# Performance work log

Hardware: AMD Instinct MI355X
Metric: run time of the kernel (lower is better)

## Reference

```python
import jax, jax.numpy as jnp
import numpy as np

N_NODES, N_EDGES, N_REL, F_DIM, N_HEAD, N_LAYERS = 20000, 100000, 1000, 128, 4, 4
NEG_SLOPE = 0.2  # PyG GATv2Conv default negative_slope


def _gatv2_layer(x, ea_full, src, dst, Wl, bl, Wr, br, We, att, bias):
    # x: [N, F]; ea_full: [Etot, F] edge attrs (incl. self-loop rows)
    N = x.shape[0]
    H, C = att.shape  # heads, out-dim per head
    xl = (x @ Wl + bl).reshape(N, H, C)          # source-side projection
    xr = (x @ Wr + br).reshape(N, H, C)          # target-side projection
    ee = (ea_full @ We).reshape(-1, H, C)        # [Etot, H, C] edge embedding
    # GATv2 scoring: leaky_relu(x_i + x_j + e) . att
    e = jax.nn.leaky_relu(xl[src] + xr[dst] + ee, NEG_SLOPE)
    logits = jnp.einsum('ehc,hc->eh', e, att)    # [Etot, H]
    # segment softmax over edges grouped by destination node
    m = jax.ops.segment_max(logits, dst, num_segments=N)
    p = jnp.exp(logits - m[dst])
    denom = jax.ops.segment_sum(p, dst, num_segments=N)
    alpha = p / denom[dst]                       # [Etot, H]
    out = jax.ops.segment_sum(alpha[:, :, None] * xl[src], dst, num_segments=N)
    return out.mean(axis=1) + bias               # concat=False -> head mean


def setup_inputs() -> dict:
    key = jax.random.key(0)
    ks = jax.random.split(key, 12)
    N, E, R, F, H, L = N_NODES, N_EDGES, N_REL, F_DIM, N_HEAD, N_LAYERS
    HC = H * F
    s = 1.0 / np.sqrt(F)
    return {
        'x': jax.random.normal(ks[0], (N, F), jnp.float32),
        'edge_index': jax.random.randint(ks[1], (2, E), 0, N, dtype=jnp.int32),
        'relations': jax.random.normal(ks[2], (R, F), jnp.float32),
        'relation_index': jax.random.randint(ks[3], (E,), 0, R, dtype=jnp.int32),
        'Wl': jax.random.normal(ks[4], (L, F, HC), jnp.float32) * s,
        'bl': jnp.zeros((L, HC), jnp.float32),
        'Wr': jax.random.normal(ks[5], (L, F, HC), jnp.float32) * s,
        'br': jnp.zeros((L, HC), jnp.float32),
        'We': jax.random.normal(ks[6], (L, F, HC), jnp.float32) * s,
        'att': jax.random.normal(ks[7], (L, H, F), jnp.float32) * s,
        'bias': jnp.zeros((L, F), jnp.float32),
    }


def reference(x, edge_index, relations, relation_index, Wl, bl, Wr, br, We, att, bias):
    N = x.shape[0]
    sl = jnp.arange(N, dtype=edge_index.dtype)
    src = jnp.concatenate([edge_index[0], sl])   # add_self_loops=True
    dst = jnp.concatenate([edge_index[1], sl])
    ea = relations[relation_index]               # [E, F]
    # self-loop edge_attr uses fill_value='mean' (PyG default)
    ea_mean = ea.mean(axis=0)
    ea_full = jnp.concatenate([ea, jnp.broadcast_to(ea_mean, (N, ea.shape[1]))])
    h = x
    for l in range(N_LAYERS):
        h = _gatv2_layer(h, ea_full, src, dst, Wl[l], bl[l], Wr[l], br[l], We[l], att[l], bias[l])
    return (h, relations)
```

## Files before the change

kernel.cpp:

```cpp
#include <hip/hip_runtime.h>
#include <hip/hip_bf16.h>

#define N_NODES   20000
#define N_EDGES   100000
#define N_REL     1000
#define F_DIM     128
#define N_HEAD    4
#define HC        512
#define HC2       256
#define N_LAYERS  4
#define REL_EXT_ROWS 1008
#define NEG_SLOPE 0.2f
#define PROJ_NODE_X 79

typedef __attribute__((ext_vector_type(8))) short short8;
typedef __attribute__((ext_vector_type(4))) float floatx4;

__device__ __forceinline__ float loadIn(const void* p, size_t i, int f32) {
    if (f32) return ((const float*)p)[i];
    union { unsigned int u; float f; } c;
    c.u = ((unsigned int)((const unsigned short*)p)[i]) << 16;
    return c.f;
}

__device__ __forceinline__ unsigned short f2bf(float v) {
    __hip_bfloat16 b = __float2bfloat16(v);
    return *(unsigned short*)&b;
}

__device__ __forceinline__ void unpack2(unsigned int u, float& lo, float& hi) {
    union { unsigned int u; float f; } a, b;
    a.u = u << 16;
    b.u = u & 0xFFFF0000u;
    lo = a.f; hi = b.f;
}

__device__ __forceinline__ void unpack8(uint4 v, float* f) {
    unpack2(v.x, f[0], f[1]);
    unpack2(v.y, f[2], f[3]);
    unpack2(v.z, f[4], f[5]);
    unpack2(v.w, f[6], f[7]);
}

__device__ __forceinline__ void gload_lds16(const unsigned short* g, short* l) {
    __builtin_amdgcn_global_load_lds(
        (const __attribute__((address_space(1))) unsigned int*)g,
        (__attribute__((address_space(3))) unsigned int*)l,
        16, 0, 0);
}

__global__ void detect_kernel(const unsigned short* __restrict__ x, int* __restrict__ flag) {
    int t = threadIdx.x;
    int cnt = 0;
    for (int j = t; j < 256; j += 64) {
        int e = (x[j] >> 7) & 0xFF;
        if (e >= 143) cnt++;
    }
    for (int off = 32; off; off >>= 1) cnt += __shfl_xor(cnt, off);
    if (t == 0) flag[0] = (cnt >= 8) ? 1 : 0;
}

__global__ void xcast_kernel(const void* __restrict__ x, unsigned short* __restrict__ xbf,
                             const int* __restrict__ flag) {
    int idx = blockIdx.x * 256 + threadIdx.x;
    if (idx >= N_NODES * F_DIM / 4) return;
    int f32 = flag[0];
    uint2 o;
    if (f32) {
        float4 v = ((const float4*)x)[idx];
        o.x = (unsigned int)f2bf(v.x) | ((unsigned int)f2bf(v.y) << 16);
        o.y = (unsigned int)f2bf(v.z) | ((unsigned int)f2bf(v.w) << 16);
    } else {
        o = ((const uint2*)x)[idx];
    }
    ((uint2*)xbf)[idx] = o;
}


__global__ void hist_kernel(const int* __restrict__ dst, const int* __restrict__ rel,
                            int* __restrict__ deg, int* __restrict__ rcount) {
    int e = blockIdx.x * 256 + threadIdx.x;
    if (e < N_EDGES) {
        atomicAdd(&deg[dst[e]], 1);
        atomicAdd(&rcount[rel[e]], 1);
    }
}

__global__ void ea_mean_kernel(const int* __restrict__ rcount,
                               const void* __restrict__ relations,
                               float* __restrict__ ea_mean, const int* __restrict__ flag) {
    int f32 = flag[0];
    int b = blockIdx.x;
    int t = threadIdx.x;
    int col = t & 127;
    int rhalf = t >> 7;
    float acc = 0.f;
    for (int j = 0; j < 4; ++j) {
        int r = b * 8 + j * 2 + rhalf;
        acc += (float)rcount[r] * loadIn(relations, (size_t)r * F_DIM + col, f32);
    }
    __shared__ float part[256];
    part[t] = acc;
    __syncthreads();
    if (t < 128)
        atomicAdd(&ea_mean[col], (part[t] + part[t + 128]) * (1.f / (float)N_EDGES));
}

__global__ void relext_kernel(const void* __restrict__ relations,
                              const float* __restrict__ ea_mean,
                              unsigned short* __restrict__ rel_ext, const int* __restrict__ flag) {
    int idx = blockIdx.x * 256 + threadIdx.x;
    if (idx >= REL_EXT_ROWS * F_DIM) return;
    int f32 = flag[0];
    int r = idx >> 7;
    int c = idx & 127;
    float v;
    if (r < N_REL)       v = loadIn(relations, idx, f32);
    else if (r == N_REL) v = ea_mean[c];
    else                 v = 0.f;
    rel_ext[idx] = f2bf(v);
}

__global__ void scan_kernel(const int* __restrict__ deg,
                            int* __restrict__ row_start, int* __restrict__ cursor) {
    __shared__ int part[1024];
    int t = threadIdx.x;
    const int CH = (N_NODES + 1023) / 1024;
    int base = t * CH;
    int sum = 0;
    for (int j = 0; j < CH; ++j) {
        int idx = base + j;
        if (idx < N_NODES) sum += deg[idx];
    }
    part[t] = sum;
    __syncthreads();
    for (int off = 1; off < 1024; off <<= 1) {
        int u = (t >= off) ? part[t - off] : 0;
        __syncthreads();
        part[t] += u;
        __syncthreads();
    }
    int run = part[t] - sum;
    for (int j = 0; j < CH; ++j) {
        int idx = base + j;
        if (idx < N_NODES) {
            row_start[idx] = run;
            cursor[idx] = run;
            run += deg[idx];
        }
    }
    if (t == 1023) row_start[N_NODES] = part[1023];
}

__global__ void scatter_kernel(const int* __restrict__ src, const int* __restrict__ dst,
                               const int* __restrict__ rel, int* __restrict__ cursor,
                               int* __restrict__ csr_pack) {
    int e = blockIdx.x * 256 + threadIdx.x;
    if (e < N_EDGES) {
        int d = dst[e];
        int p = atomicAdd(&cursor[d], 1);
        csr_pack[p] = src[e] | (rel[e] << 16);
    }
}

__global__ void build8_kernel(const int* __restrict__ row_start,
                              const int* __restrict__ csr_pack,
                              int* __restrict__ csr8) {
    int i = blockIdx.x * 256 + threadIdx.x;
    if (i >= N_NODES) return;
    int rs = row_start[i];
    int deg = row_start[i + 1] - rs;
    if (deg < 0) deg = 0;
    int dcap = deg > 4095 ? 4095 : deg;
    csr8[i * 8] = rs | (dcap << 17);
    #pragma unroll
    for (int k = 0; k < 7; ++k)
        csr8[i * 8 + 1 + k] = (k < deg) ? csr_pack[rs + k] : 0;
}

__global__ void tail_kernel(const void* __restrict__ relations, void* __restrict__ out,
                            const int* __restrict__ flag) {
    int i = blockIdx.x * 256 + threadIdx.x;
    if (i >= N_REL * F_DIM) return;
    int f32 = flag[0];
    float v = loadIn(relations, i, f32);
    size_t o = (size_t)N_NODES * F_DIM + i;
    if (f32) ((float*)out)[o] = v;
    else     ((unsigned short*)out)[o] = f2bf(v);
}

__global__ void w_transpose_kernel(const void* __restrict__ Wl, const void* __restrict__ Wr,
                                   const void* __restrict__ We,
                                   unsigned short* __restrict__ Wt, const int* __restrict__ flag) {
    int f32 = flag[0];
    int k0 = blockIdx.x * 64;
    int n0 = blockIdx.y * 64;
    int mat = blockIdx.z;
    const void* src = (mat < 4) ? Wl : (mat < 8 ? Wr : We);
    size_t base = (size_t)(mat & 3) * F_DIM * HC;
    unsigned short* dst = Wt + (size_t)mat * HC * F_DIM;
    __shared__ float T[64][65];
    int t = threadIdx.x;
    int r = t >> 2, cq = t & 3;
    for (int j = 0; j < 16; ++j) {
        int n = cq * 16 + j;
        T[n][r] = loadIn(src, base + (size_t)(k0 + r) * HC + n0 + n, f32);
    }
    __syncthreads();
    for (int j = 0; j < 16; ++j) {
        int k = cq * 16 + j;
        dst[(size_t)(n0 + r) * F_DIM + k0 + k] = f2bf(T[r][k]);
    }
}

__launch_bounds__(256, 2)
__global__ void proj_kernel(const unsigned short* __restrict__ A_node,
                            const unsigned short* __restrict__ rel_ext,
                            const unsigned short* __restrict__ Wlt,
                            const unsigned short* __restrict__ Wrt,
                            const unsigned short* __restrict__ Wet,
                            const void* __restrict__ bl, const void* __restrict__ br,
                            size_t boff,
                            unsigned short* __restrict__ xl,
                            unsigned short* __restrict__ xr,
                            unsigned short* __restrict__ re,
                            const int* __restrict__ flag) {
    __shared__ __align__(16) short As[2][64 * 128];
    __shared__ __align__(16) short Cw[4][32][72];
    int f32 = flag[0];
    int t = threadIdx.x;
    int y = blockIdx.y;
    int isNode = (blockIdx.x < PROJ_NODE_X);

    const unsigned short* A;
    const unsigned short* WtM[2];
    const void* biasM[2];
    unsigned short* outM[2];
    int M, mbase, n0M[2];
    if (isNode) {
        A = A_node; M = N_NODES;
        mbase = blockIdx.x * 256;
        WtM[0] = Wlt;  WtM[1] = Wrt;
        biasM[0] = bl; biasM[1] = br;
        outM[0] = xl;  outM[1] = xr;
        n0M[0] = y * 128; n0M[1] = y * 128;
    } else {
        A = rel_ext; M = REL_EXT_ROWS;
        int s = (blockIdx.x - PROJ_NODE_X) * 4 + y;
        mbase = (s >> 1) * 256;
        WtM[0] = Wet;  WtM[1] = Wet;
        biasM[0] = nullptr; biasM[1] = nullptr;
        outM[0] = re;  outM[1] = re;
        n0M[0] = (s & 1) * 256; n0M[1] = (s & 1) * 256 + 128;
    }
    const int nT = 4;

    int wave = t >> 6, lane = t & 63;
    int wm = (wave >> 1) * 32, wn = (wave & 1) * 64;
    int r16 = lane & 15, quad = lane >> 4;

    short8 breg[2][2][2][4];
    #pragma unroll
    for (int m = 0; m < 2; ++m)
        #pragma unroll
        for (int half = 0; half < 2; ++half)
            #pragma unroll
            for (int kk = 0; kk < 2; ++kk)
                #pragma unroll
                for (int ni = 0; ni < 4; ++ni)
                    breg[m][half][kk][ni] = *(const short8*)(
                        WtM[m] + (size_t)(n0M[m] + wn + ni * 16 + r16) * F_DIM
                               + half * 64 + kk * 32 + quad * 8);

    float bvv[2][4];
    #pragma unroll
    for (int m = 0; m < 2; ++m)
        #pragma unroll
        for (int ni = 0; ni < 4; ++ni)
            bvv[m][ni] = biasM[m] ? loadIn(biasM[m], boff + n0M[m] + wn + ni * 16 + r16, f32) : 0.f;

    auto STAGE = [&](int buf, int ct2) {
        int base = mbase + ct2 * 64;
        #pragma unroll
        for (int j = 0; j < 4; ++j) {
            int c = t + j * 256;
            int row = c >> 4, ch = c & 15;
            int gm = base + row;
            if (gm >= M) gm = M - 1;
            int sch = ch ^ (row & 15);
            gload_lds16(A + (size_t)gm * F_DIM + sch * 8, &As[buf][c * 8]);
        }
    };

    STAGE(0, 0);
    asm volatile("s_waitcnt vmcnt(0)" ::: "memory");
    __builtin_amdgcn_sched_barrier(0);
    __syncthreads();

    int cur = 0;
    for (int ct = 0; ct < nT; ++ct) {
        int m0 = mbase + ct * 64;
        if (ct + 1 < nT) STAGE(cur ^ 1, ct + 1);
        __builtin_amdgcn_sched_barrier(0);

        short8 afr[2][2][2];
        #pragma unroll
        for (int half = 0; half < 2; ++half)
            #pragma unroll
            for (int kk = 0; kk < 2; ++kk)
                #pragma unroll
                for (int mi = 0; mi < 2; ++mi) {
                    int row = wm + mi * 16 + r16;
                    int pch = (half * 8 + kk * 4 + quad) ^ (row & 15);
                    afr[half][kk][mi] = *(const short8*)&As[cur][row * 128 + pch * 8];
                }

        #pragma unroll
        for (int m = 0; m < 2; ++m) {
            floatx4 acc[2][4];
            #pragma unroll
            for (int mi = 0; mi < 2; ++mi)
                #pragma unroll
                for (int ni = 0; ni < 4; ++ni)
                    acc[mi][ni] = (floatx4){0.f, 0.f, 0.f, 0.f};

            #pragma unroll
            for (int half = 0; half < 2; ++half)
                #pragma unroll
                for (int kk = 0; kk < 2; ++kk)
                    #pragma unroll
                    for (int mi = 0; mi < 2; ++mi)
                        #pragma unroll
                        for (int ni = 0; ni < 4; ++ni)
                            acc[mi][ni] = __builtin_amdgcn_mfma_f32_16x16x32_bf16(
                                afr[half][kk][mi], breg[m][half][kk][ni], acc[mi][ni], 0, 0, 0);

            #pragma unroll
            for (int mi = 0; mi < 2; ++mi)
                #pragma unroll
                for (int ni = 0; ni < 4; ++ni)
                    #pragma unroll
                    for (int r = 0; r < 4; ++r)
                        Cw[wave][mi * 16 + quad * 4 + r][ni * 16 + r16] =
                            (short)f2bf(acc[mi][ni][r] + bvv[m][ni]);
            asm volatile("s_waitcnt lgkmcnt(0)" ::: "memory");
            __builtin_amdgcn_sched_barrier(0);

            unsigned short* out = outM[m];
            #pragma unroll
            for (int j = 0; j < 4; ++j) {
                int c = j * 64 + lane;
                int lr = c >> 3, chunk = c & 7;
                int gm = m0 + wm + lr;
                if (gm >= M) gm = M - 1;
                *(short8*)(out + (size_t)gm * HC + n0M[m] + wn + chunk * 8) =
                    *(const short8*)&Cw[wave][lr][chunk * 8];
            }
        }

        if (ct + 1 < nT) {
            asm volatile("s_waitcnt vmcnt(8)" ::: "memory");
            __builtin_amdgcn_sched_barrier(0);
        }
        __builtin_amdgcn_s_barrier();
        cur ^= 1;
    }
}

__launch_bounds__(128)
__global__ void edge_kernel(const unsigned int* __restrict__ xl2,
                            const unsigned int* __restrict__ xr2,
                            const unsigned int* __restrict__ re2,
                            const int* __restrict__ csr8,
                            const int* __restrict__ csr_pack,
                            const void* __restrict__ att, size_t att_off,
                            const void* __restrict__ bias, size_t bias_off,
                            void* __restrict__ hout, int final_layer,
                            const int* __restrict__ flag) {
    int f32 = flag[0];
    int wid = threadIdx.x >> 6;
    int lane = threadIdx.x & 63;
    int i = blockIdx.x * 2 + wid;
    if (i >= N_NODES) return;
    int h = lane >> 4;
    int q = lane & 15;
    int loff = h * 64 + q * 4;

    uint4 h0 = *(const uint4*)(csr8 + (size_t)i * 8);
    uint4 h1 = *(const uint4*)(csr8 + (size_t)i * 8 + 4);
    int rs  = (int)(h0.x & 0x1FFFF);
    int deg = (int)(h0.x >> 17) & 0xFFF;
    int ew[7] = { (int)h0.y, (int)h0.z, (int)h0.w, (int)h1.x, (int)h1.y, (int)h1.z, (int)h1.w };

    float xr[8];
    { uint4 v = *(const uint4*)(xr2 + (size_t)i * HC2 + loff); unpack8(v, xr); }
    float er[8];
    { uint4 v = *(const uint4*)(re2 + (size_t)N_REL * HC2 + loff); unpack8(v, er); }
    float av[8];
    #pragma unroll
    for (int j = 0; j < 8; ++j)
        av[j] = loadIn(att, att_off + (size_t)h * F_DIM + q * 8 + j, f32);

    int nIn = deg > 7 ? 7 : deg;
    uint4 xv[7], rv[7];
    #pragma unroll
    for (int k = 0; k < 7; ++k) {
        if (k < nIn) {
            int pk = ew[k];
            int sn = pk & 0xFFFF;        if (sn >= N_NODES) sn = 0;
            int rn = (pk >> 16) & 0x3FF; if (rn > N_REL) rn = N_REL;
            xv[k] = *(const uint4*)(xl2 + (size_t)sn * HC2 + loff);
            rv[k] = *(const uint4*)(re2 + (size_t)rn * HC2 + loff);
        }
    }

    float acc[8];
    float s;
    {
        float xs[8];
        uint4 v = *(const uint4*)(xl2 + (size_t)i * HC2 + loff);
        unpack8(v, xs);
        float part = 0.f;
        #pragma unroll
        for (int j = 0; j < 8; ++j) {
            float u = xs[j] + xr[j] + er[j];
            u = fmaxf(u, NEG_SLOPE * u);
            part = fmaf(u, av[j], part);
        }
        #pragma unroll
        for (int off = 8; off; off >>= 1) part += __shfl_xor(part, off);
        part = fminf(fmaxf(part, -60.f), 60.f);
        float p = __expf(part);
        s = p;
        #pragma unroll
        for (int j = 0; j < 8; ++j) acc[j] = p * xs[j];
    }

    #pragma unroll
    for (int k = 0; k < 7; ++k) {
        if (k < nIn) {
            float xlv[8], ee[8];
            unpack8(xv[k], xlv);
            unpack8(rv[k], ee);
            float part = 0.f;
            #pragma unroll
            for (int j = 0; j < 8; ++j) {
                float u = xlv[j] + xr[j] + ee[j];
                u = fmaxf(u, NEG_SLOPE * u);
                part = fmaf(u, av[j], part);
            }
            #pragma unroll
            for (int off = 8; off; off >>= 1) part += __shfl_xor(part, off);
            part = fminf(fmaxf(part, -60.f), 60.f);
            float pp = __expf(part);
            s += pp;
            #pragma unroll
            for (int j = 0; j < 8; ++j) acc[j] = fmaf(pp, xlv[j], acc[j]);
        }
    }

    if (deg > 7) {
        int e1 = rs + deg;
        if (e1 > N_EDGES) e1 = N_EDGES;
        for (int b = rs + 7; b < e1; b += 4) {
            int nb = e1 - b; if (nb > 4) nb = 4;
            uint4 xo[4], ro[4];
            #pragma unroll
            for (int k = 0; k < 4; ++k) {
                if (k < nb) {
                    int pk = csr_pack[b + k];
                    int sn = pk & 0xFFFF;        if (sn >= N_NODES) sn = 0;
                    int rn = (pk >> 16) & 0x3FF; if (rn > N_REL) rn = N_REL;
                    xo[k] = *(const uint4*)(xl2 + (size_t)sn * HC2 + loff);
                    ro[k] = *(const uint4*)(re2 + (size_t)rn * HC2 + loff);
                }
            }
            #pragma unroll
            for (int k = 0; k < 4; ++k) {
                if (k < nb) {
                    float xlv[8], ee[8];
                    unpack8(xo[k], xlv);
                    unpack8(ro[k], ee);
                    float part = 0.f;
                    #pragma unroll
                    for (int j = 0; j < 8; ++j) {
                        float u = xlv[j] + xr[j] + ee[j];
                        u = fmaxf(u, NEG_SLOPE * u);
                        part = fmaf(u, av[j], part);
                    }
                    #pragma unroll
                    for (int off = 8; off; off >>= 1) part += __shfl_xor(part, off);
                    part = fminf(fmaxf(part, -60.f), 60.f);
                    float pp = __expf(part);
                    s += pp;
                    #pragma unroll
                    for (int j = 0; j < 8; ++j) acc[j] = fmaf(pp, xlv[j], acc[j]);
                }
            }
        }
    }

    float inv = 1.f / s;
    float outv[8];
    #pragma unroll
    for (int j = 0; j < 8; ++j) outv[j] = acc[j] * inv;
    #pragma unroll
    for (int j = 0; j < 8; ++j) {
        outv[j] += __shfl_xor(outv[j], 16);
        outv[j] += __shfl_xor(outv[j], 32);
    }

    if (h == 0) {
        float bv[8];
        #pragma unroll
        for (int j = 0; j < 8; ++j)
            bv[j] = loadIn(bias, bias_off + q * 8 + j, f32);
        size_t o = (size_t)i * F_DIM + q * 8;
        if (final_layer && f32) {
            float* op = (float*)hout + o;
            float4 lo, hi;
            lo.x = outv[0] * 0.25f + bv[0];
            lo.y = outv[1] * 0.25f + bv[1];
            lo.z = outv[2] * 0.25f + bv[2];
            lo.w = outv[3] * 0.25f + bv[3];
            hi.x = outv[4] * 0.25f + bv[4];
            hi.y = outv[5] * 0.25f + bv[5];
            hi.z = outv[6] * 0.25f + bv[6];
            hi.w = outv[7] * 0.25f + bv[7];
            *(float4*)op = lo;
            *(float4*)(op + 4) = hi;
        } else {
            unsigned int w[4];
            #pragma unroll
            for (int p = 0; p < 4; ++p) {
                float v0 = outv[2 * p] * 0.25f + bv[2 * p];
                float v1 = outv[2 * p + 1] * 0.25f + bv[2 * p + 1];
                w[p] = (unsigned int)f2bf(v0) | ((unsigned int)f2bf(v1) << 16);
            }
            *(uint4*)((unsigned short*)hout + o) = *(uint4*)w;
        }
    }
}


extern "C" void kernel_launch(void* const* d_in, const int* in_sizes, int n_in,
                              void* d_out, int out_size, void* d_ws, size_t ws_size,
                              hipStream_t stream) {
    const void* x          = d_in[0];
    const int*  edge_index = (const int*)d_in[1];
    const void* relations  = d_in[2];
    const int*  rel_index  = (const int*)d_in[3];
    const void* Wl         = d_in[4];
    const void* bl         = d_in[5];
    const void* Wr         = d_in[6];
    const void* br         = d_in[7];
    const void* We         = d_in[8];
    const void* att        = d_in[9];
    const void* bias       = d_in[10];

    char* ws = (char*)d_ws;
    size_t off = 0;
    auto alloc = [&](size_t bytes) -> void* {
        void* p = ws + off;
        off = (off + bytes + 255) & ~(size_t)255;
        return p;
    };
    int*            flag     = (int*)alloc(4);
    char*           zero0    = ws + off;
    int*            deg      = (int*)alloc(N_NODES * 4);
    int*            rcount   = (int*)alloc(N_REL * 4);
    float*          ea_mean  = (float*)alloc(F_DIM * 4);
    size_t          zlen     = (size_t)((ws + off) - zero0);
    int*            row_start= (int*)alloc((N_NODES + 1) * 4);
    int*            cursor   = (int*)alloc(N_NODES * 4);
    int*            csr_pack = (int*)alloc(N_EDGES * 4);
    int*            csr8     = (int*)alloc((size_t)N_NODES * 8 * 4);
    unsigned short* rel_ext  = (unsigned short*)alloc((size_t)REL_EXT_ROWS * F_DIM * 2);
    unsigned short* xbf      = (unsigned short*)alloc((size_t)N_NODES * F_DIM * 2);
    unsigned short* Wt       = (unsigned short*)alloc((size_t)12 * HC * F_DIM * 2);
    unsigned short* re       = (unsigned short*)alloc((size_t)REL_EXT_ROWS * HC * 2);
    unsigned short* hbuf     = (unsigned short*)alloc((size_t)N_NODES * F_DIM * 2);
    unsigned short* xl       = (unsigned short*)alloc((size_t)N_NODES * HC * 2);
    unsigned short* xr       = (unsigned short*)alloc((size_t)N_NODES * HC * 2);

    const int* esrc = edge_index;
    const int* edst = edge_index + N_EDGES;

    detect_kernel<<<1, 64, 0, stream>>>((const unsigned short*)x, flag);
    hipMemsetAsync(zero0, 0, zlen, stream);
    xcast_kernel<<<(N_NODES * F_DIM / 4 + 255) / 256, 256, 0, stream>>>(x, xbf, flag);
    hist_kernel<<<(N_EDGES + 255) / 256, 256, 0, stream>>>(edst, rel_index, deg, rcount);
    ea_mean_kernel<<<N_REL / 8, 256, 0, stream>>>(rcount, relations, ea_mean, flag);
    relext_kernel<<<(REL_EXT_ROWS * F_DIM + 255) / 256, 256, 0, stream>>>(relations, ea_mean, rel_ext, flag);
    scan_kernel<<<1, 1024, 0, stream>>>(deg, row_start, cursor);
    scatter_kernel<<<(N_EDGES + 255) / 256, 256, 0, stream>>>(esrc, edst, rel_index, cursor, csr_pack);
    build8_kernel<<<(N_NODES + 255) / 256, 256, 0, stream>>>(row_start, csr_pack, csr8);
    w_transpose_kernel<<<dim3(2, 8, 12), 256, 0, stream>>>(Wl, Wr, We, Wt, flag);
    tail_kernel<<<(N_REL * F_DIM + 255) / 256, 256, 0, stream>>>(relations, d_out, flag);

    const unsigned short* hin = xbf;
    for (int l = 0; l < N_LAYERS; ++l) {
        const unsigned short* Wlt = Wt + (size_t)l * HC * F_DIM;
        const unsigned short* Wrt = Wt + (size_t)(4 + l) * HC * F_DIM;
        const unsigned short* Wet = Wt + (size_t)(8 + l) * HC * F_DIM;
        proj_kernel<<<dim3(PROJ_NODE_X + 2, 4), 256, 0, stream>>>(
            hin, rel_ext, Wlt, Wrt, Wet,
            bl, br, (size_t)l * HC,
            xl, xr, re, flag);
        int final_layer = (l == N_LAYERS - 1);
        void* hout = final_layer ? d_out : (void*)hbuf;
        edge_kernel<<<(N_NODES + 1) / 2, 128, 0, stream>>>(
            (const unsigned int*)xl, (const unsigned int*)xr, (const unsigned int*)re,
            csr8, csr_pack,
            att, (size_t)l * N_HEAD * F_DIM,
            bias, (size_t)l * F_DIM,
            hout, final_layer, flag);
        hin = hbuf;
    }
}
```

Before: 420.1 us.

## Fuse setup kernels into one launch and halve projection tile rows for more blocks

Merges histogram, relation-tail copy, input cast and weight transpose into a single prep kernel dispatched by block index, cutting launch count. Changes the projection kernel to process 128 rows per block with twice as many blocks, improving occupancy and load balance across CUs. Also removes an explicit LDS wait before reading back the staging tile, relying on compiler-inserted waits. Smaller tiles reduce per-block weight reuse of preloaded B registers.

New measurement: 418.4 us. No clear change (-0.4%).

```diff
diff --git a/kernel.cpp b/kernel.cpp
--- a/kernel.cpp
+++ b/kernel.cpp
@@ -11,7 +11,13 @@
 #define N_LAYERS  4
 #define REL_EXT_ROWS 1008
 #define NEG_SLOPE 0.2f
-#define PROJ_NODE_X 79
+#define PROJ_NODE_X 157
+
+#define HIST_B   ((N_EDGES + 255) / 256)
+#define TAIL_B   ((N_REL * F_DIM + 255) / 256)
+#define XCAST_B  ((N_NODES * F_DIM / 4 + 255) / 256)
+#define WT_B     (2 * 8 * 12)
+#define PREP_B   (HIST_B + TAIL_B + XCAST_B + WT_B)
 
 typedef __attribute__((ext_vector_type(8))) short short8;
 typedef __attribute__((ext_vector_type(4))) float floatx4;
@@ -60,31 +66,74 @@
     if (t == 0) flag[0] = (cnt >= 8) ? 1 : 0;
 }
 
-__global__ void xcast_kernel(const void* __restrict__ x, unsigned short* __restrict__ xbf,
-                             const int* __restrict__ flag) {
-    int idx = blockIdx.x * 256 + threadIdx.x;
-    if (idx >= N_NODES * F_DIM / 4) return;
+__global__ void prep_kernel(const int* __restrict__ dst, const int* __restrict__ rel,
+                            int* __restrict__ deg, int* __restrict__ rcount,
+                            const void* __restrict__ relations, void* __restrict__ out,
+                            const void* __restrict__ x, unsigned short* __restrict__ xbf,
+                            const void* __restrict__ Wl, const void* __restrict__ Wr,
+                            const void* __restrict__ We, unsigned short* __restrict__ Wt,
+                            const int* __restrict__ flag) {
+    __shared__ float T[64][65];
     int f32 = flag[0];
-    uint2 o;
-    if (f32) {
-        float4 v = ((const float4*)x)[idx];
-        o.x = (unsigned int)f2bf(v.x) | ((unsigned int)f2bf(v.y) << 16);
-        o.y = (unsigned int)f2bf(v.z) | ((unsigned int)f2bf(v.w) << 16);
-    } else {
-        o = ((const uint2*)x)[idx];
-    }
-    ((uint2*)xbf)[idx] = o;
-}
-
-
-__global__ void hist_kernel(const int* __restrict__ dst, const int* __restrict__ rel,
-                            int* __restrict__ deg, int* __restrict__ rcount) {
-    int e = blockIdx.x * 256 + threadIdx.x;
-    if (e < N_EDGES) {
-        atomicAdd(&deg[dst[e]], 1);
-        atomicAdd(&rcount[rel[e]], 1);
-    }
-}
+    int b = blockIdx.x;
+    int t = threadIdx.x;
+    if (b < HIST_B) {
+        int e = b * 256 + t;
+        if (e < N_EDGES) {
+            atomicAdd(&deg[dst[e]], 1);
+            atomicAdd(&rcount[rel[e]], 1);
+        }
+        return;
+    }
+    b -= HIST_B;
+    if (b < TAIL_B) {
+        int i = b * 256 + t;
+        if (i < N_REL * F_DIM) {
+            float v = loadIn(relations, i, f32);
+            size_t o = (size_t)N_NODES * F_DIM + i;
+            if (f32) ((float*)out)[o] = v;
+            else     ((unsigned short*)out)[o] = f2bf(v);
+        }
+        return;
+    }
+    b -= TAIL_B;
+    if (b < XCAST_B) {
+        int idx = b * 256 + t;
+        if (idx < N_NODES * F_DIM / 4) {
+            uint2 o;
+            if (f32) {
+                float4 v = ((const float4*)x)[idx];
+                o.x = (unsigned int)f2bf(v.x) | ((unsigned int)f2bf(v.y) << 16);
+                o.y = (unsigned int)f2bf(v.z) | ((unsigned int)f2bf(v.w) << 16);
+            } else {
+                o = ((const uint2*)x)[idx];
+            }
+            ((uint2*)xbf)[idx] = o;
+        }
+        return;
+    }
+    b -= XCAST_B;
+    {
+        int mat = b >> 4;
+        int rem = b & 15;
+        int n0 = (rem >> 1) * 64;
+        int k0 = (rem & 1) * 64;
+        const void* src = (mat < 4) ? Wl : (mat < 8 ? Wr : We);
+        size_t base = (size_t)(mat & 3) * F_DIM * HC;
+        unsigned short* dstp = Wt + (size_t)mat * HC * F_DIM;
+        int r = t >> 2, cq = t & 3;
+        for (int j = 0; j < 16; ++j) {
+            int n = cq * 16 + j;
+            T[n][r] = loadIn(src, base + (size_t)(k0 + r) * HC + n0 + n, f32);
+        }
+        __syncthreads();
+        for (int j = 0; j < 16; ++j) {
+            int k = cq * 16 + j;
+            dstp[(size_t)(n0 + r) * F_DIM + k0 + k] = f2bf(T[r][k]);
+        }
+    }
+}
+
 
 __global__ void ea_mean_kernel(const int* __restrict__ rcount,
                                const void* __restrict__ relations,
@@ -176,41 +225,6 @@
     #pragma unroll
     for (int k = 0; k < 7; ++k)
         csr8[i * 8 + 1 + k] = (k < deg) ? csr_pack[rs + k] : 0;
-}
-
-__global__ void tail_kernel(const void* __restrict__ relations, void* __restrict__ out,
-                            const int* __restrict__ flag) {
-    int i = blockIdx.x * 256 + threadIdx.x;
-    if (i >= N_REL * F_DIM) return;
-    int f32 = flag[0];
-    float v = loadIn(relations, i, f32);
-    size_t o = (size_t)N_NODES * F_DIM + i;
-    if (f32) ((float*)out)[o] = v;
-    else     ((unsigned short*)out)[o] = f2bf(v);
-}
-
-__global__ void w_transpose_kernel(const void* __restrict__ Wl, const void* __restrict__ Wr,
-                                   const void* __restrict__ We,
-                                   unsigned short* __restrict__ Wt, const int* __restrict__ flag) {
-    int f32 = flag[0];
-    int k0 = blockIdx.x * 64;
-    int n0 = blockIdx.y * 64;
-    int mat = blockIdx.z;
-    const void* src = (mat < 4) ? Wl : (mat < 8 ? Wr : We);
-    size_t base = (size_t)(mat & 3) * F_DIM * HC;
-    unsigned short* dst = Wt + (size_t)mat * HC * F_DIM;
-    __shared__ float T[64][65];
-    int t = threadIdx.x;
-    int r = t >> 2, cq = t & 3;
-    for (int j = 0; j < 16; ++j) {
-        int n = cq * 16 + j;
-        T[n][r] = loadIn(src, base + (size_t)(k0 + r) * HC + n0 + n, f32);
-    }
-    __syncthreads();
-    for (int j = 0; j < 16; ++j) {
-        int k = cq * 16 + j;
-        dst[(size_t)(n0 + r) * F_DIM + k0 + k] = f2bf(T[r][k]);
-    }
 }
 
 __launch_bounds__(256, 2)
@@ -239,7 +253,7 @@
     int M, mbase, n0M[2];
     if (isNode) {
         A = A_node; M = N_NODES;
-        mbase = blockIdx.x * 256;
+        mbase = blockIdx.x * 128;
         WtM[0] = Wlt;  WtM[1] = Wrt;
         biasM[0] = bl; biasM[1] = br;
         outM[0] = xl;  outM[1] = xr;
@@ -247,13 +261,13 @@
     } else {
         A = rel_ext; M = REL_EXT_ROWS;
         int s = (blockIdx.x - PROJ_NODE_X) * 4 + y;
-        mbase = (s >> 1) * 256;
+        mbase = (s >> 1) * 128;
         WtM[0] = Wet;  WtM[1] = Wet;
         biasM[0] = nullptr; biasM[1] = nullptr;
         outM[0] = re;  outM[1] = re;
         n0M[0] = (s & 1) * 256; n0M[1] = (s & 1) * 256 + 128;
     }
-    const int nT = 4;
+    const int nT = 2;
 
     int wave = t >> 6, lane = t & 63;
     int wm = (wave >> 1) * 32, wn = (wave & 1) * 64;
@@ -343,8 +357,6 @@
                     for (int r = 0; r < 4; ++r)
                         Cw[wave][mi * 16 + quad * 4 + r][ni * 16 + r16] =
                             (short)f2bf(acc[mi][ni][r] + bvv[m][ni]);
-            asm volatile("s_waitcnt lgkmcnt(0)" ::: "memory");
-            __builtin_amdgcn_sched_barrier(0);
 
             unsigned short* out = outM[m];
             #pragma unroll
@@ -588,22 +600,21 @@
 
     detect_kernel<<<1, 64, 0, stream>>>((const unsigned short*)x, flag);
     hipMemsetAsync(zero0, 0, zlen, stream);
-    xcast_kernel<<<(N_NODES * F_DIM / 4 + 255) / 256, 256, 0, stream>>>(x, xbf, flag);
-    hist_kernel<<<(N_EDGES + 255) / 256, 256, 0, stream>>>(edst, rel_index, deg, rcount);
+    prep_kernel<<<PREP_B, 256, 0, stream>>>(edst, rel_index, deg, rcount,
+                                            relations, d_out, x, xbf,
+                                            Wl, Wr, We, Wt, flag);
     ea_mean_kernel<<<N_REL / 8, 256, 0, stream>>>(rcount, relations, ea_mean, flag);
+    scan_kernel<<<1, 1024, 0, stream>>>(deg, row_start, cursor);
     relext_kernel<<<(REL_EXT_ROWS * F_DIM + 255) / 256, 256, 0, stream>>>(relations, ea_mean, rel_ext, flag);
-    scan_kernel<<<1, 1024, 0, stream>>>(deg, row_start, cursor);
     scatter_kernel<<<(N_EDGES + 255) / 256, 256, 0, stream>>>(esrc, edst, rel_index, cursor, csr_pack);
     build8_kernel<<<(N_NODES + 255) / 256, 256, 0, stream>>>(row_start, csr_pack, csr8);
-    w_transpose_kernel<<<dim3(2, 8, 12), 256, 0, stream>>>(Wl, Wr, We, Wt, flag);
-    tail_kernel<<<(N_REL * F_DIM + 255) / 256, 256, 0, stream>>>(relations, d_out, flag);
 
     const unsigned short* hin = xbf;
     for (int l = 0; l < N_LAYERS; ++l) {
         const unsigned short* Wlt = Wt + (size_t)l * HC * F_DIM;
         const unsigned short* Wrt = Wt + (size_t)(4 + l) * HC * F_DIM;
         const unsigned short* Wet = Wt + (size_t)(8 + l) * HC * F_DIM;
-        proj_kernel<<<dim3(PROJ_NODE_X + 2, 4), 256, 0, stream>>>(
+        proj_kernel<<<dim3(PROJ_NODE_X + 4, 4), 256, 0, stream>>>(
             hin, rel_ext, Wlt, Wrt, Wet,
             bl, br, (size_t)l * HC,
             xl, xr, re, flag);
```
